# Kernel tuning notes

Measured on AMD Instinct MI355X. Metric: run time of the kernel, lower is better.

## Reference

```python
import jax, jax.numpy as jnp
import numpy as np

DIM = 1024
HEADS = 16
DIM_HEAD = 64
INNER = HEADS * DIM_HEAD
SCALE = DIM_HEAD ** -0.5
LN_EPS = 1e-5
MASK_VALUE = -np.finfo(np.float32).max


def setup_inputs() -> dict:
    key = jax.random.key(0)
    ks = jax.random.split(key, 3)
    x = jax.random.normal(ks[0], (2, 2048, DIM), dtype=jnp.float32)
    w_qkv = jax.random.normal(ks[1], (DIM, 3 * INNER), dtype=jnp.float32) * (DIM ** -0.5)
    w_out = jax.random.normal(ks[2], (INNER, DIM), dtype=jnp.float32) * (INNER ** -0.5)
    ln_gamma = jnp.ones((DIM,), dtype=jnp.float32)
    ln_beta = jnp.zeros((DIM,), dtype=jnp.float32)
    return {"x": x, "ln_gamma": ln_gamma, "ln_beta": ln_beta, "w_qkv": w_qkv, "w_out": w_out}


def reference(x, ln_gamma, ln_beta, w_qkv, w_out):
    b, n, _ = x.shape
    # LayerNorm
    mu = jnp.mean(x, axis=-1, keepdims=True)
    var = jnp.mean(jnp.square(x - mu), axis=-1, keepdims=True)
    xn = (x - mu) * jax.lax.rsqrt(var + LN_EPS) * ln_gamma + ln_beta
    # QKV projection, split into heads: b n (h d) -> b h n d
    qkv = xn @ w_qkv  # [b, n, 3*inner]
    q, k, v = jnp.split(qkv, 3, axis=-1)
    def to_heads(t):
        return t.reshape(b, n, HEADS, DIM_HEAD).transpose(0, 2, 1, 3)
    q, k, v = to_heads(q), to_heads(k), to_heads(v)
    # scaled scores with diagonal excluded
    dots = jnp.einsum('bhnd,bhmd->bhnm', q, k) * SCALE
    eye = jnp.eye(n, dtype=bool)
    dots = jnp.where(eye, MASK_VALUE, dots)
    attn = jax.nn.softmax(dots, axis=-1)
    out = jnp.einsum('bhnm,bhmd->bhnd', attn, v)
    out = out.transpose(0, 2, 1, 3).reshape(b, n, INNER)
    return out @ w_out
```

## Files before the change

kernel.cpp:

```cpp
#include <hip/hip_runtime.h>


#define DIMM   1024
#define NSEQ   2048
#define BATCH  2
#define HEADS  16
#define DHEAD  64
#define QKVN   3072
#define MROWS  4096

typedef float          f32x4  __attribute__((ext_vector_type(4)));
typedef __bf16         bf16x8 __attribute__((ext_vector_type(8)));
typedef __bf16         bf16x4 __attribute__((ext_vector_type(4)));
typedef unsigned short u16x8  __attribute__((ext_vector_type(8)));
typedef unsigned short u16x4  __attribute__((ext_vector_type(4)));

#define QSCALE (0.125f * 1.4426950408889634f)

#if __has_builtin(__builtin_amdgcn_exp2f)
#define EXP2(x) __builtin_amdgcn_exp2f(x)
#else
#define EXP2(x) exp2f(x)
#endif

__device__ __forceinline__ unsigned short f2bf(float f) {
  unsigned u = __builtin_bit_cast(unsigned, f);
  u += 0x7FFFu + ((u >> 16) & 1u);
  return (unsigned short)(u >> 16);
}
__device__ __forceinline__ bf16x8 as_bf(u16x8 v) { return __builtin_bit_cast(bf16x8, v); }

__device__ __forceinline__ u16x4 cvt4(f32x4 v) {
  bf16x4 b;
  b[0] = (__bf16)v[0]; b[1] = (__bf16)v[1]; b[2] = (__bf16)v[2]; b[3] = (__bf16)v[3];
  return __builtin_bit_cast(u16x4, b);
}

__device__ __forceinline__ void gl_lds16(const unsigned short* g, unsigned short* l) {
  __builtin_amdgcn_global_load_lds(
      (const __attribute__((address_space(1))) unsigned*)g,
      (__attribute__((address_space(3))) unsigned*)l, 16, 0, 0);
}

__device__ __forceinline__ bf16x8 lds_frag(const unsigned short* base, int row, int chunk) {
  return as_bf(*(const u16x8*)&base[row * 64 + ((chunk ^ (row & 7)) << 3)]);
}

__device__ __forceinline__ void transpose_tile(
    const float* __restrict__ src, unsigned short* __restrict__ dst,
    int R, int C, int bx, int by, int tid) {
  __shared__ float t[32][33];
  const int rb = by * 32, cb = bx * 32;
  const int r0 = tid >> 5;
  const int c  = tid & 31;
#pragma unroll
  for (int i = 0; i < 4; ++i)
    t[r0 + i * 8][c] = src[(rb + r0 + i * 8) * C + cb + c];
  __syncthreads();
#pragma unroll
  for (int i = 0; i < 4; ++i)
    dst[(cb + r0 + i * 8) * R + rb + c] = f2bf(t[c][r0 + i * 8]);
}

__global__ __launch_bounds__(256) void prep_kernel(
    const float* __restrict__ x, const float* __restrict__ g,
    const float* __restrict__ be, const float* __restrict__ w_qkv,
    const float* __restrict__ w_out, unsigned short* __restrict__ xn,
    unsigned short* __restrict__ wqkvT, unsigned short* __restrict__ woutT) {
  const int bid = blockIdx.x, tid = threadIdx.x;
  if (bid < MROWS) {
    const int row = bid;
    const int wave = tid >> 6, lane = tid & 63;
    const float4 v = *(const float4*)&x[row * DIMM + tid * 4];
    float s  = v.x + v.y + v.z + v.w;
    float s2 = v.x * v.x + v.y * v.y + v.z * v.z + v.w * v.w;
#pragma unroll
    for (int o = 32; o >= 1; o >>= 1) { s += __shfl_xor(s, o); s2 += __shfl_xor(s2, o); }
    __shared__ float ps[4], ps2[4];
    if (lane == 0) { ps[wave] = s; ps2[wave] = s2; }
    __syncthreads();
    s  = ps[0] + ps[1] + ps[2] + ps[3];
    s2 = ps2[0] + ps2[1] + ps2[2] + ps2[3];
    const float mu  = s * (1.0f / DIMM);
    const float var = s2 * (1.0f / DIMM) - mu * mu;
    const float rs  = rsqrtf(var + 1e-5f);
    const float4 gg = *(const float4*)&g[tid * 4];
    const float4 bb = *(const float4*)&be[tid * 4];
    u16x4 o;
    o[0] = f2bf((v.x - mu) * rs * gg.x + bb.x);
    o[1] = f2bf((v.y - mu) * rs * gg.y + bb.y);
    o[2] = f2bf((v.z - mu) * rs * gg.z + bb.z);
    o[3] = f2bf((v.w - mu) * rs * gg.w + bb.w);
    *(u16x4*)&xn[row * DIMM + tid * 4] = o;
  } else {
    const int t = bid - MROWS;
    const int bx = t & 127, by = t >> 7;
    if (bx < QKVN / 32) transpose_tile(w_qkv, wqkvT, DIMM, QKVN, bx, by, tid);
    else                transpose_tile(w_out, woutT, DIMM, DIMM, bx - QKVN / 32, by, tid);
  }
}

__global__ __launch_bounds__(256, 3) void gemm_qkv_kernel(
    const unsigned short* __restrict__ A, const unsigned short* __restrict__ Bt,
    unsigned short* __restrict__ qb, unsigned short* __restrict__ kb,
    unsigned short* __restrict__ vtb) {
  __shared__ __attribute__((aligned(16))) unsigned short As[128 * 64];
  __shared__ __attribute__((aligned(16))) unsigned short Bs[128 * 64];
  const int tid = threadIdx.x;
  const int bm = blockIdx.y, bn = blockIdx.x;
  const int lane = tid & 63, wave = tid >> 6;
  const int l15 = lane & 15, quad = lane >> 4;
  const int wm = wave >> 1, wn = wave & 1;
  const int lrow = lane >> 3;
  const int gcol = ((lane & 7) ^ lrow) << 3;
  const unsigned short* Ab = A  + (bm * 128 + wave * 32 + lrow) * DIMM + gcol;
  const unsigned short* Bb = Bt + (bn * 128 + wave * 32 + lrow) * DIMM + gcol;
  const bool swap = (bn < 16);
  f32x4 acc[4][4] = {};

  for (int k0 = 0; k0 < DIMM; k0 += 64) {
#pragma unroll
    for (int j = 0; j < 4; ++j) {
      gl_lds16(Ab + j * 8 * DIMM + k0, &As[(wave * 32 + j * 8) * 64]);
      gl_lds16(Bb + j * 8 * DIMM + k0, &Bs[(wave * 32 + j * 8) * 64]);
    }
    __syncthreads();
#pragma unroll
    for (int kk = 0; kk < 2; ++kk) {
      bf16x8 af[4], bfr[4];
#pragma unroll
      for (int mi = 0; mi < 4; ++mi) af[mi]  = lds_frag(As, wm * 64 + mi * 16 + l15, kk * 4 + quad);
#pragma unroll
      for (int ni = 0; ni < 4; ++ni) bfr[ni] = lds_frag(Bs, wn * 64 + ni * 16 + l15, kk * 4 + quad);
      if (swap) {
#pragma unroll
        for (int mi = 0; mi < 4; ++mi)
#pragma unroll
          for (int ni = 0; ni < 4; ++ni)
            acc[mi][ni] = __builtin_amdgcn_mfma_f32_16x16x32_bf16(bfr[ni], af[mi], acc[mi][ni], 0, 0, 0);
      } else {
#pragma unroll
        for (int mi = 0; mi < 4; ++mi)
#pragma unroll
          for (int ni = 0; ni < 4; ++ni)
            acc[mi][ni] = __builtin_amdgcn_mfma_f32_16x16x32_bf16(af[mi], bfr[ni], acc[mi][ni], 0, 0, 0);
      }
    }
    __syncthreads();
  }

  if (swap) {
    const int colbase = bn * 128 + wn * 64;
    const int which = colbase >> 10;
    unsigned short* dst = which ? kb : qb;
    const float sc = which ? 1.0f : QSCALE;
#pragma unroll
    for (int mi = 0; mi < 4; ++mi) {
      const int m = bm * 128 + wm * 64 + mi * 16 + l15;
      const int bh0 = (m >> 11) * HEADS;
      const int n = m & 2047;
#pragma unroll
      for (int ni = 0; ni < 4; ++ni) {
        const int wc = (colbase & 1023) + ni * 16 + quad * 4;
        const int h = wc >> 6, dd = wc & 63;
        f32x4 v = acc[mi][ni] * sc;
        *(u16x4*)&dst[((bh0 + h) * NSEQ + n) * DHEAD + dd] = cvt4(v);
      }
    }
  } else {
    const int colbase = bn * 128 + wn * 64 - 2048;
#pragma unroll
    for (int mi = 0; mi < 4; ++mi) {
      const int m0 = bm * 128 + wm * 64 + mi * 16 + quad * 4;
      const int bh0 = (m0 >> 11) * HEADS;
      const int n0 = m0 & 2047;
#pragma unroll
      for (int ni = 0; ni < 4; ++ni) {
        const int vcol = colbase + ni * 16 + l15;
        const int h = vcol >> 6, dd = vcol & 63;
        *(u16x4*)&vtb[((bh0 + h) * DHEAD + dd) * NSEQ + n0] = cvt4(acc[mi][ni]);
      }
    }
  }
}

__global__ __launch_bounds__(256, 2) void attn_kernel(
    const unsigned short* __restrict__ qb, const unsigned short* __restrict__ kb,
    const unsigned short* __restrict__ vtb, unsigned short* __restrict__ attn_out) {
  __shared__ __attribute__((aligned(16))) unsigned short Ks[2][64 * 64];
  __shared__ __attribute__((aligned(16))) unsigned short Vts[2][64 * 64];
  __shared__ __attribute__((aligned(16))) unsigned short Ps[4][16][72];
  const int tid = threadIdx.x, wave = tid >> 6, lane = tid & 63;
  const int l15 = lane & 15, quad = lane >> 4;
  const int bh = blockIdx.x, qt = blockIdx.y;
  const int b = bh >> 4, h = bh & 15;
  const int qbase = qt * 256 + wave * 64;

  bf16x8 aq[4][2];
#pragma unroll
  for (int sub = 0; sub < 4; ++sub) {
    const unsigned short* qrow = qb + (bh * NSEQ + qbase + sub * 16 + l15) * DHEAD;
    aq[sub][0] = as_bf(*(const u16x8*)(qrow + quad * 8));
    aq[sub][1] = as_bf(*(const u16x8*)(qrow + 32 + quad * 8));
  }

  float lsum[4] = {};
  f32x4 occ[4][4] = {};

  const int lrow = lane >> 3;
  const int gcol = ((lane & 7) ^ lrow) << 3;
  const unsigned short* Kb = kb  + (bh * NSEQ + wave * 16 + lrow) * DHEAD + gcol;
  const unsigned short* Vb = vtb + (bh * DHEAD + wave * 16 + lrow) * NSEQ + gcol;

  gl_lds16(Kb,             &Ks[0][(wave * 16) * 64]);
  gl_lds16(Kb + 8 * DHEAD, &Ks[0][(wave * 16 + 8) * 64]);
  gl_lds16(Vb,             &Vts[0][(wave * 16) * 64]);
  gl_lds16(Vb + 8 * NSEQ,  &Vts[0][(wave * 16 + 8) * 64]);

  const int diag_it = qt * 4 + wave;
  const bool diag_lane = ((l15 >> 2) == quad);
  const int diag_r = l15 & 3;

  for (int it = 0; it < NSEQ / 64; ++it) {
    const int cur = it & 1;
    __syncthreads();
    if (it < NSEQ / 64 - 1) {
      gl_lds16(Kb + (it + 1) * 64 * DHEAD,             &Ks[cur ^ 1][(wave * 16) * 64]);
      gl_lds16(Kb + (it + 1) * 64 * DHEAD + 8 * DHEAD, &Ks[cur ^ 1][(wave * 16 + 8) * 64]);
      gl_lds16(Vb + (it + 1) * 64,                     &Vts[cur ^ 1][(wave * 16) * 64]);
      gl_lds16(Vb + (it + 1) * 64 + 8 * NSEQ,          &Vts[cur ^ 1][(wave * 16 + 8) * 64]);
    }
    bf16x8 ak[2][4], av[2][4];
#pragma unroll
    for (int kk = 0; kk < 2; ++kk)
#pragma unroll
      for (int ct = 0; ct < 4; ++ct) {
        ak[kk][ct] = lds_frag(&Ks[cur][0],  ct * 16 + l15, kk * 4 + quad);
        av[kk][ct] = lds_frag(&Vts[cur][0], ct * 16 + l15, kk * 4 + quad);
      }
#pragma unroll
    for (int sub = 0; sub < 4; ++sub) {
      f32x4 scc[4];
#pragma unroll
      for (int ct = 0; ct < 4; ++ct) scc[ct] = (f32x4){-32.f, -32.f, -32.f, -32.f};
#pragma unroll
      for (int kk = 0; kk < 2; ++kk)
#pragma unroll
        for (int ct = 0; ct < 4; ++ct)
          scc[ct] = __builtin_amdgcn_mfma_f32_16x16x32_bf16(ak[kk][ct], aq[sub][kk], scc[ct], 0, 0, 0);
#pragma unroll
      for (int ct = 0; ct < 4; ++ct)
#pragma unroll
        for (int r = 0; r < 4; ++r) scc[ct][r] = EXP2(scc[ct][r]);

      if (it == diag_it && diag_lane) scc[sub][diag_r] = 0.f;

      f32x4 ps4 = (scc[0] + scc[1]) + (scc[2] + scc[3]);
      lsum[sub] += (ps4[0] + ps4[1]) + (ps4[2] + ps4[3]);

#pragma unroll
      for (int ct = 0; ct < 4; ++ct)
        *(u16x4*)&Ps[wave][l15][ct * 16 + quad * 4] = cvt4(scc[ct]);

#pragma unroll
      for (int kk = 0; kk < 2; ++kk) {
        bf16x8 bp = as_bf(*(const u16x8*)&Ps[wave][l15][kk * 32 + quad * 8]);
#pragma unroll
        for (int ct = 0; ct < 4; ++ct)
          occ[sub][ct] = __builtin_amdgcn_mfma_f32_16x16x32_bf16(av[kk][ct], bp, occ[sub][ct], 0, 0, 0);
      }
    }
  }
#pragma unroll
  for (int sub = 0; sub < 4; ++sub) {
    float l = lsum[sub];
    l += __shfl_xor(l, 16);
    l += __shfl_xor(l, 32);
    const float rl = __builtin_amdgcn_rcpf(l);
    const int qg = qbase + sub * 16 + l15;
#pragma unroll
    for (int ct = 0; ct < 4; ++ct) {
      f32x4 ov = occ[sub][ct] * rl;
      *(u16x4*)&attn_out[(b * NSEQ + qg) * DIMM + h * DHEAD + ct * 16 + quad * 4] = cvt4(ov);
    }
  }
}

__global__ __launch_bounds__(256, 2) void gemm_out_kernel(
    const unsigned short* __restrict__ A,
    const unsigned short* __restrict__ Bt,
    float* __restrict__ out) {
  __shared__ __attribute__((aligned(16))) unsigned short As[2 * 64 * 64];
  __shared__ __attribute__((aligned(16))) unsigned short Bs[2 * 128 * 64];
  const int tid = threadIdx.x;
  const int bm = blockIdx.y, bn = blockIdx.x;
  const int lane = tid & 63, wave = tid >> 6;
  const int l15 = lane & 15, quad = lane >> 4;
  const int wm = wave >> 1, wn = wave & 1;
  const int lrow = lane >> 3;
  const int gcol = ((lane & 7) ^ lrow) << 3;
  const unsigned short* Ab = A  + (bm * 64 + wave * 16 + lrow) * DIMM + gcol;
  const unsigned short* Bb = Bt + (bn * 128 + wave * 32 + lrow) * DIMM + gcol;
  f32x4 acc[2][4] = {};

#pragma unroll
  for (int j = 0; j < 2; ++j) gl_lds16(Ab + j * 8 * DIMM, &As[(wave * 16 + j * 8) * 64]);
#pragma unroll
  for (int j = 0; j < 4; ++j) gl_lds16(Bb + j * 8 * DIMM, &Bs[(wave * 32 + j * 8) * 64]);

  for (int it = 0; it < DIMM / 64; ++it) {
    const int cur = it & 1;
    __syncthreads();
    if (it < DIMM / 64 - 1) {
      const int k0 = (it + 1) * 64;
      unsigned short* An = &As[(cur ^ 1) * 4096];
      unsigned short* Bn = &Bs[(cur ^ 1) * 8192];
#pragma unroll
      for (int j = 0; j < 2; ++j) gl_lds16(Ab + j * 8 * DIMM + k0, &An[(wave * 16 + j * 8) * 64]);
#pragma unroll
      for (int j = 0; j < 4; ++j) gl_lds16(Bb + j * 8 * DIMM + k0, &Bn[(wave * 32 + j * 8) * 64]);
    }
    const unsigned short* Ac = &As[cur * 4096];
    const unsigned short* Bc = &Bs[cur * 8192];
#pragma unroll
    for (int kk = 0; kk < 2; ++kk) {
      bf16x8 af[2], bfr[4];
#pragma unroll
      for (int mi = 0; mi < 2; ++mi) af[mi]  = lds_frag(Ac, wm * 32 + mi * 16 + l15, kk * 4 + quad);
#pragma unroll
      for (int ni = 0; ni < 4; ++ni) bfr[ni] = lds_frag(Bc, wn * 64 + ni * 16 + l15, kk * 4 + quad);
#pragma unroll
      for (int mi = 0; mi < 2; ++mi)
#pragma unroll
        for (int ni = 0; ni < 4; ++ni)
          acc[mi][ni] = __builtin_amdgcn_mfma_f32_16x16x32_bf16(bfr[ni], af[mi], acc[mi][ni], 0, 0, 0);
    }
  }
#pragma unroll
  for (int mi = 0; mi < 2; ++mi) {
    const int m = bm * 64 + wm * 32 + mi * 16 + l15;
#pragma unroll
    for (int ni = 0; ni < 4; ++ni) {
      const int col = bn * 128 + wn * 64 + ni * 16 + quad * 4;
      *(f32x4*)&out[m * DIMM + col] = acc[mi][ni];
    }
  }
}

extern "C" void kernel_launch(void* const* d_in, const int* in_sizes, int n_in,
                              void* d_out, int out_size, void* d_ws, size_t ws_size,
                              hipStream_t stream) {
  const float* x     = (const float*)d_in[0];
  const float* gamma = (const float*)d_in[1];
  const float* beta  = (const float*)d_in[2];
  const float* w_qkv = (const float*)d_in[3];
  const float* w_out = (const float*)d_in[4];
  float* out = (float*)d_out;

  char* ws = (char*)d_ws;
  unsigned short* xn    = (unsigned short*)(ws);
  unsigned short* wqkvT = (unsigned short*)(ws + 8388608);
  unsigned short* woutT = (unsigned short*)(ws + 14680064);
  unsigned short* qbuf  = (unsigned short*)(ws + 16777216);
  unsigned short* kbuf  = (unsigned short*)(ws + 25165824);
  unsigned short* vtbuf = (unsigned short*)(ws + 33554432);
  unsigned short* attnb = (unsigned short*)(ws + 41943040);

  prep_kernel<<<MROWS + (QKVN + DIMM) / 32 * (DIMM / 32), 256, 0, stream>>>(
      x, gamma, beta, w_qkv, w_out, xn, wqkvT, woutT);
  gemm_qkv_kernel<<<dim3(24, MROWS / 128), 256, 0, stream>>>(xn, wqkvT, qbuf, kbuf, vtbuf);
  attn_kernel<<<dim3(BATCH * HEADS, NSEQ / 256), 256, 0, stream>>>(qbuf, kbuf, vtbuf, attnb);
  gemm_out_kernel<<<dim3(DIMM / 128, MROWS / 64), 256, 0, stream>>>(attnb, woutT, out);
}
```

Before: 201.1 us.

## Split attention KV range across two blocks and merge with combine kernel

```diff
diff --git a/kernel.cpp b/kernel.cpp
--- a/kernel.cpp
+++ b/kernel.cpp
@@ -186,13 +186,15 @@
 
 __global__ __launch_bounds__(256, 2) void attn_kernel(
     const unsigned short* __restrict__ qb, const unsigned short* __restrict__ kb,
-    const unsigned short* __restrict__ vtb, unsigned short* __restrict__ attn_out) {
+    const unsigned short* __restrict__ vtb,
+    unsigned short* __restrict__ o0, unsigned short* __restrict__ o1,
+    float* __restrict__ lws) {
   __shared__ __attribute__((aligned(16))) unsigned short Ks[2][64 * 64];
   __shared__ __attribute__((aligned(16))) unsigned short Vts[2][64 * 64];
   __shared__ __attribute__((aligned(16))) unsigned short Ps[4][16][72];
   const int tid = threadIdx.x, wave = tid >> 6, lane = tid & 63;
   const int l15 = lane & 15, quad = lane >> 4;
-  const int bh = blockIdx.x, qt = blockIdx.y;
+  const int bh = blockIdx.x, qt = blockIdx.y, half = blockIdx.z;
   const int b = bh >> 4, h = bh & 15;
   const int qbase = qt * 256 + wave * 64;
 
@@ -212,19 +214,21 @@
   const unsigned short* Kb = kb  + (bh * NSEQ + wave * 16 + lrow) * DHEAD + gcol;
   const unsigned short* Vb = vtb + (bh * DHEAD + wave * 16 + lrow) * NSEQ + gcol;
 
-  gl_lds16(Kb,             &Ks[0][(wave * 16) * 64]);
-  gl_lds16(Kb + 8 * DHEAD, &Ks[0][(wave * 16 + 8) * 64]);
-  gl_lds16(Vb,             &Vts[0][(wave * 16) * 64]);
-  gl_lds16(Vb + 8 * NSEQ,  &Vts[0][(wave * 16 + 8) * 64]);
+  const int it0 = half * 16, it1 = it0 + 16;
+
+  gl_lds16(Kb + it0 * 64 * DHEAD,             &Ks[0][(wave * 16) * 64]);
+  gl_lds16(Kb + it0 * 64 * DHEAD + 8 * DHEAD, &Ks[0][(wave * 16 + 8) * 64]);
+  gl_lds16(Vb + it0 * 64,                     &Vts[0][(wave * 16) * 64]);
+  gl_lds16(Vb + it0 * 64 + 8 * NSEQ,          &Vts[0][(wave * 16 + 8) * 64]);
 
   const int diag_it = qt * 4 + wave;
   const bool diag_lane = ((l15 >> 2) == quad);
   const int diag_r = l15 & 3;
 
-  for (int it = 0; it < NSEQ / 64; ++it) {
+  for (int it = it0; it < it1; ++it) {
     const int cur = it & 1;
     __syncthreads();
-    if (it < NSEQ / 64 - 1) {
+    if (it < it1 - 1) {
       gl_lds16(Kb + (it + 1) * 64 * DHEAD,             &Ks[cur ^ 1][(wave * 16) * 64]);
       gl_lds16(Kb + (it + 1) * 64 * DHEAD + 8 * DHEAD, &Ks[cur ^ 1][(wave * 16 + 8) * 64]);
       gl_lds16(Vb + (it + 1) * 64,                     &Vts[cur ^ 1][(wave * 16) * 64]);
@@ -271,19 +275,40 @@
       }
     }
   }
+  unsigned short* odst = half ? o1 : o0;
+  float* ldst = lws + half * (32 * NSEQ);
 #pragma unroll
   for (int sub = 0; sub < 4; ++sub) {
     float l = lsum[sub];
     l += __shfl_xor(l, 16);
     l += __shfl_xor(l, 32);
-    const float rl = __builtin_amdgcn_rcpf(l);
     const int qg = qbase + sub * 16 + l15;
-#pragma unroll
-    for (int ct = 0; ct < 4; ++ct) {
-      f32x4 ov = occ[sub][ct] * rl;
-      *(u16x4*)&attn_out[(b * NSEQ + qg) * DIMM + h * DHEAD + ct * 16 + quad * 4] = cvt4(ov);
-    }
-  }
+    if (quad == 0) ldst[bh * NSEQ + qg] = l;
+#pragma unroll
+    for (int ct = 0; ct < 4; ++ct)
+      *(u16x4*)&odst[(b * NSEQ + qg) * DIMM + h * DHEAD + ct * 16 + quad * 4] = cvt4(occ[sub][ct]);
+  }
+}
+
+__global__ __launch_bounds__(256) void combine_kernel(
+    const unsigned short* __restrict__ o0, unsigned short* __restrict__ o1,
+    const float* __restrict__ lws) {
+  const int idx4 = blockIdx.x * 256 + threadIdx.x;
+  const int flat = idx4 * 4;
+  const int row = flat >> 10;
+  const int col = flat & 1023;
+  const int bhq = ((row >> 11) * HEADS + (col >> 6)) * NSEQ + (row & 2047);
+  const float rl = __builtin_amdgcn_rcpf(lws[bhq] + lws[32 * NSEQ + bhq]);
+  const u16x4 a = *(const u16x4*)&o0[flat];
+  const u16x4 b = *(const u16x4*)&o1[flat];
+  f32x4 s;
+#pragma unroll
+  for (int i = 0; i < 4; ++i) {
+    const float fa = __builtin_bit_cast(float, (unsigned)a[i] << 16);
+    const float fb = __builtin_bit_cast(float, (unsigned)b[i] << 16);
+    s[i] = (fa + fb) * rl;
+  }
+  *(u16x4*)&o1[flat] = cvt4(s);
 }
 
 __global__ __launch_bounds__(256, 2) void gemm_out_kernel(
@@ -365,10 +390,14 @@
   unsigned short* kbuf  = (unsigned short*)(ws + 25165824);
   unsigned short* vtbuf = (unsigned short*)(ws + 33554432);
   unsigned short* attnb = (unsigned short*)(ws + 41943040);
+  unsigned short* o0    = xn;
+  unsigned short* o1    = attnb;
+  float*          lws   = (float*)(ws + 8388608);
 
   prep_kernel<<<MROWS + (QKVN + DIMM) / 32 * (DIMM / 32), 256, 0, stream>>>(
       x, gamma, beta, w_qkv, w_out, xn, wqkvT, woutT);
   gemm_qkv_kernel<<<dim3(24, MROWS / 128), 256, 0, stream>>>(xn, wqkvT, qbuf, kbuf, vtbuf);
-  attn_kernel<<<dim3(BATCH * HEADS, NSEQ / 256), 256, 0, stream>>>(qbuf, kbuf, vtbuf, attnb);
+  attn_kernel<<<dim3(BATCH * HEADS, NSEQ / 256, 2), 256, 0, stream>>>(qbuf, kbuf, vtbuf, o0, o1, lws);
+  combine_kernel<<<MROWS * DIMM / 4 / 256, 256, 0, stream>>>(o0, o1, lws);
   gemm_out_kernel<<<dim3(DIMM / 128, MROWS / 64), 256, 0, stream>>>(attnb, woutT, out);
 }
```

After: 193.2 us. -3.9%, faster.

## Split attention key loop four ways with atomic fp32 accumulation and combine pass

Applied to the files above, without the earlier changes.

```diff
diff --git a/kernel.cpp b/kernel.cpp
--- a/kernel.cpp
+++ b/kernel.cpp
@@ -184,16 +184,24 @@
   }
 }
 
-__global__ __launch_bounds__(256, 2) void attn_kernel(
+__global__ __launch_bounds__(256) void zero_kernel(
+    float* __restrict__ oacc, float* __restrict__ lacc) {
+  const int bid = blockIdx.x, tid = threadIdx.x;
+  const f32x4 z = {0.f, 0.f, 0.f, 0.f};
+  if (bid < 4096) *(f32x4*)&oacc[(bid * 256 + tid) * 4] = z;
+  else            *(f32x4*)&lacc[((bid - 4096) * 256 + tid) * 4] = z;
+}
+
+__global__ __launch_bounds__(256, 4) void attn_kernel(
     const unsigned short* __restrict__ qb, const unsigned short* __restrict__ kb,
-    const unsigned short* __restrict__ vtb, unsigned short* __restrict__ attn_out) {
-  __shared__ __attribute__((aligned(16))) unsigned short Ks[2][64 * 64];
-  __shared__ __attribute__((aligned(16))) unsigned short Vts[2][64 * 64];
+    const unsigned short* __restrict__ vtb,
+    float* __restrict__ oacc, float* __restrict__ lacc) {
+  __shared__ __attribute__((aligned(16))) unsigned short Ks[64 * 64];
+  __shared__ __attribute__((aligned(16))) unsigned short Vts[64 * 64];
   __shared__ __attribute__((aligned(16))) unsigned short Ps[4][16][72];
   const int tid = threadIdx.x, wave = tid >> 6, lane = tid & 63;
   const int l15 = lane & 15, quad = lane >> 4;
-  const int bh = blockIdx.x, qt = blockIdx.y;
-  const int b = bh >> 4, h = bh & 15;
+  const int bh = blockIdx.x, qt = blockIdx.y, z = blockIdx.z;
   const int qbase = qt * 256 + wave * 64;
 
   bf16x8 aq[4][2];
@@ -212,31 +220,26 @@
   const unsigned short* Kb = kb  + (bh * NSEQ + wave * 16 + lrow) * DHEAD + gcol;
   const unsigned short* Vb = vtb + (bh * DHEAD + wave * 16 + lrow) * NSEQ + gcol;
 
-  gl_lds16(Kb,             &Ks[0][(wave * 16) * 64]);
-  gl_lds16(Kb + 8 * DHEAD, &Ks[0][(wave * 16 + 8) * 64]);
-  gl_lds16(Vb,             &Vts[0][(wave * 16) * 64]);
-  gl_lds16(Vb + 8 * NSEQ,  &Vts[0][(wave * 16 + 8) * 64]);
+  const int it0 = z * 8, it1 = it0 + 8;
 
   const int diag_it = qt * 4 + wave;
   const bool diag_lane = ((l15 >> 2) == quad);
   const int diag_r = l15 & 3;
 
-  for (int it = 0; it < NSEQ / 64; ++it) {
-    const int cur = it & 1;
-    __syncthreads();
-    if (it < NSEQ / 64 - 1) {
-      gl_lds16(Kb + (it + 1) * 64 * DHEAD,             &Ks[cur ^ 1][(wave * 16) * 64]);
-      gl_lds16(Kb + (it + 1) * 64 * DHEAD + 8 * DHEAD, &Ks[cur ^ 1][(wave * 16 + 8) * 64]);
-      gl_lds16(Vb + (it + 1) * 64,                     &Vts[cur ^ 1][(wave * 16) * 64]);
-      gl_lds16(Vb + (it + 1) * 64 + 8 * NSEQ,          &Vts[cur ^ 1][(wave * 16 + 8) * 64]);
-    }
+  for (int it = it0; it < it1; ++it) {
+    gl_lds16(Kb + it * 64 * DHEAD,             &Ks[(wave * 16) * 64]);
+    gl_lds16(Kb + it * 64 * DHEAD + 8 * DHEAD, &Ks[(wave * 16 + 8) * 64]);
+    gl_lds16(Vb + it * 64,                     &Vts[(wave * 16) * 64]);
+    gl_lds16(Vb + it * 64 + 8 * NSEQ,          &Vts[(wave * 16 + 8) * 64]);
+    __syncthreads();
+
     bf16x8 ak[2][4], av[2][4];
 #pragma unroll
     for (int kk = 0; kk < 2; ++kk)
 #pragma unroll
       for (int ct = 0; ct < 4; ++ct) {
-        ak[kk][ct] = lds_frag(&Ks[cur][0],  ct * 16 + l15, kk * 4 + quad);
-        av[kk][ct] = lds_frag(&Vts[cur][0], ct * 16 + l15, kk * 4 + quad);
+        ak[kk][ct] = lds_frag(Ks,  ct * 16 + l15, kk * 4 + quad);
+        av[kk][ct] = lds_frag(Vts, ct * 16 + l15, kk * 4 + quad);
       }
 #pragma unroll
     for (int sub = 0; sub < 4; ++sub) {
@@ -270,19 +273,47 @@
           occ[sub][ct] = __builtin_amdgcn_mfma_f32_16x16x32_bf16(av[kk][ct], bp, occ[sub][ct], 0, 0, 0);
       }
     }
-  }
+    __syncthreads();
+  }
+  float* obase = oacc + (size_t)bh * 64 * NSEQ;
 #pragma unroll
   for (int sub = 0; sub < 4; ++sub) {
     float l = lsum[sub];
     l += __shfl_xor(l, 16);
     l += __shfl_xor(l, 32);
-    const float rl = __builtin_amdgcn_rcpf(l);
     const int qg = qbase + sub * 16 + l15;
-#pragma unroll
-    for (int ct = 0; ct < 4; ++ct) {
-      f32x4 ov = occ[sub][ct] * rl;
-      *(u16x4*)&attn_out[(b * NSEQ + qg) * DIMM + h * DHEAD + ct * 16 + quad * 4] = cvt4(ov);
-    }
+    if (quad == 0) atomicAdd(&lacc[bh * NSEQ + qg], l);
+#pragma unroll
+    for (int ct = 0; ct < 4; ++ct)
+#pragma unroll
+      for (int r = 0; r < 4; ++r)
+        atomicAdd(&obase[(ct * 16 + quad * 4 + r) * NSEQ + qg], occ[sub][ct][r]);
+  }
+}
+
+__global__ __launch_bounds__(256) void combine_kernel(
+    const float* __restrict__ oacc, const float* __restrict__ lacc,
+    unsigned short* __restrict__ attnb) {
+  __shared__ float Ls[64][65];
+  __shared__ float Lr[64];
+  const int bh = blockIdx.x, qt = blockIdx.y;
+  const int b = bh >> 4, h = bh & 15;
+  const int tid = threadIdx.x;
+  const int tq = tid & 63, td = tid >> 6;
+  const int q0 = qt * 64;
+  const float* src = oacc + (size_t)bh * 64 * NSEQ + q0;
+  if (tid < 64) Lr[tid] = lacc[bh * NSEQ + q0 + tid];
+#pragma unroll
+  for (int i = 0; i < 16; ++i) {
+    const int d = td * 16 + i;
+    Ls[d][tq] = src[d * NSEQ + tq];
+  }
+  __syncthreads();
+#pragma unroll
+  for (int i = 0; i < 16; ++i) {
+    const int q = td * 16 + i;
+    const float rl = __builtin_amdgcn_rcpf(Lr[q]);
+    attnb[(b * NSEQ + q0 + q) * DIMM + h * DHEAD + tq] = f2bf(Ls[tq][q] * rl);
   }
 }
 
@@ -360,15 +391,19 @@
   char* ws = (char*)d_ws;
   unsigned short* xn    = (unsigned short*)(ws);
   unsigned short* wqkvT = (unsigned short*)(ws + 8388608);
-  unsigned short* woutT = (unsigned short*)(ws + 14680064);
   unsigned short* qbuf  = (unsigned short*)(ws + 16777216);
   unsigned short* kbuf  = (unsigned short*)(ws + 25165824);
   unsigned short* vtbuf = (unsigned short*)(ws + 33554432);
-  unsigned short* attnb = (unsigned short*)(ws + 41943040);
+  unsigned short* woutT = (unsigned short*)(ws + 41943040);
+  float*          oacc  = (float*)(ws);
+  float*          lacc  = (float*)(ws + 44040192);
+  unsigned short* attnb = qbuf;
 
   prep_kernel<<<MROWS + (QKVN + DIMM) / 32 * (DIMM / 32), 256, 0, stream>>>(
       x, gamma, beta, w_qkv, w_out, xn, wqkvT, woutT);
   gemm_qkv_kernel<<<dim3(24, MROWS / 128), 256, 0, stream>>>(xn, wqkvT, qbuf, kbuf, vtbuf);
-  attn_kernel<<<dim3(BATCH * HEADS, NSEQ / 256), 256, 0, stream>>>(qbuf, kbuf, vtbuf, attnb);
+  zero_kernel<<<4096 + 64, 256, 0, stream>>>(oacc, lacc);
+  attn_kernel<<<dim3(BATCH * HEADS, NSEQ / 256, 4), 256, 0, stream>>>(qbuf, kbuf, vtbuf, oacc, lacc);
+  combine_kernel<<<dim3(BATCH * HEADS, NSEQ / 64), 256, 0, stream>>>(oacc, lacc, attnb);
   gemm_out_kernel<<<dim3(DIMM / 128, MROWS / 64), 256, 0, stream>>>(attnb, woutT, out);
 }
```

Result: slower. 474.5 us (+136.0%).
